# Kernel optimization log

Measured on AMD Instinct MI355X. Metric: run time of the kernel, lower is better.

Reference implementation:

```python
import jax, jax.numpy as jnp
import numpy as np

N_HEAD = 16
N_KV_HEAD = 4
HEAD_DIM = 64
VE_CH = 12  # min(12, n_embd)


def apply_rotary_emb(x, cos, sin):
    d = x.shape[3] // 2
    x1, x2 = x[..., :d], x[..., d:]
    return jnp.concatenate([x1 * cos + x2 * sin, x1 * -sin + x2 * cos], axis=3)


def rms_norm(x):
    return x * jax.lax.rsqrt(jnp.mean(jnp.square(x), axis=-1, keepdims=True) + 1e-6)


def setup_inputs() -> dict:
    key = jax.random.key(0)
    ks = jax.random.split(key, 9)
    B, T, C = 2, 2048, 1024
    s = 0.02
    return {
        "x": jax.random.normal(ks[0], (B, T, C), jnp.float32),
        "ve": jax.random.normal(ks[1], (B, T, N_KV_HEAD * HEAD_DIM), jnp.float32),
        "cos": jax.random.normal(ks[2], (1, T, 1, HEAD_DIM // 2), jnp.float32),
        "sin": jax.random.normal(ks[3], (1, T, 1, HEAD_DIM // 2), jnp.float32),
        "Wq": jax.random.normal(ks[4], (C, C), jnp.float32) * s,
        "Wk": jax.random.normal(ks[5], (N_KV_HEAD * HEAD_DIM, C), jnp.float32) * s,
        "Wv": jax.random.normal(ks[6], (N_KV_HEAD * HEAD_DIM, C), jnp.float32) * s,
        "Wo": jax.random.normal(ks[7], (C, C), jnp.float32) * s,
        "Wg": jax.random.normal(ks[8], (N_KV_HEAD, VE_CH), jnp.float32) * s,
    }


def reference(x, ve, cos, sin, Wq, Wk, Wv, Wo, Wg):
    B, T, C = x.shape
    q = (x @ Wq.T).reshape(B, T, N_HEAD, HEAD_DIM)
    k = (x @ Wk.T).reshape(B, T, N_KV_HEAD, HEAD_DIM)
    v = (x @ Wv.T).reshape(B, T, N_KV_HEAD, HEAD_DIM)

    # value-embedding gate
    ve_r = ve.reshape(B, T, N_KV_HEAD, HEAD_DIM)
    gate = 3.0 * jax.nn.sigmoid(x[..., :VE_CH] @ Wg.T)  # [B,T,n_kv_head]
    v = v + gate[..., None] * ve_r

    q = apply_rotary_emb(q, cos, sin)
    k = apply_rotary_emb(k, cos, sin)
    q = rms_norm(q) * 1.2
    k = rms_norm(k) * 1.2

    # GQA: expand kv heads
    r = N_HEAD // N_KV_HEAD
    k = jnp.repeat(k, r, axis=2)
    v = jnp.repeat(v, r, axis=2)

    # [B,H,T,D]
    q = q.transpose(0, 2, 1, 3)
    k = k.transpose(0, 2, 1, 3)
    v = v.transpose(0, 2, 1, 3)

    scale = 1.0 / np.sqrt(HEAD_DIM).astype(np.float32)
    scores = jnp.einsum("bhqd,bhkd->bhqk", q, k) * scale
    causal = jnp.tril(jnp.ones((T, T), dtype=bool))
    scores = jnp.where(causal, scores, jnp.float32(-jnp.inf))
    att = jax.nn.softmax(scores, axis=-1)
    y = jnp.einsum("bhqk,bhkd->bhqd", att, v)
    y = y.transpose(0, 2, 1, 3).reshape(B, T, C)
    return y @ Wo.T
```

## Files before the change

### kernel.cpp

```cpp
#include <hip/hip_runtime.h>
#include <stdint.h>

#define B_SZ 2
#define T_SZ 2048
#define C_SZ 1024
#define NH   16
#define NKV  4
#define HD   64
#define KVD  256
#define QKV_N 1536

typedef __attribute__((ext_vector_type(8))) short bf16x8;
typedef __attribute__((ext_vector_type(4))) float f32x4;

#define GL(p) ((const __attribute__((address_space(1))) void*)(p))
#define LD(p) ((__attribute__((address_space(3))) void*)(p))

__device__ inline unsigned short f2bf(float f) {
  union { float f; unsigned u; } v; v.f = f;
  unsigned u = v.u;
  unsigned r = (u + 0x7fffu + ((u >> 16) & 1u)) >> 16;
  return (unsigned short)r;
}
__device__ inline unsigned short bftrunc(float f) {
  union { float f; unsigned u; } v; v.f = f;
  return (unsigned short)(v.u >> 16);
}

struct Cvt5 {
  const float *s0, *s1, *s2, *s3, *s4;
  unsigned short *d0, *d1, *d2, *d3, *d4;
};
__global__ __launch_bounds__(256) void cvt_all(Cvt5 a) {
  int blk = blockIdx.x, tid = threadIdx.x;
  const float* s; unsigned short* d; int i;
  if      (blk < 4096) { s = a.s0; d = a.d0; i = blk * 256 + tid; }
  else if (blk < 5120) { s = a.s1; d = a.d1; i = (blk - 4096) * 256 + tid; }
  else if (blk < 5376) { s = a.s2; d = a.d2; i = (blk - 5120) * 256 + tid; }
  else if (blk < 5632) { s = a.s3; d = a.d3; i = (blk - 5376) * 256 + tid; }
  else                 { s = a.s4; d = a.d4; i = (blk - 5632) * 256 + tid; }
  float4 f = ((const float4*)s)[i];
  ushort4 o;
  o.x = f2bf(f.x); o.y = f2bf(f.y); o.z = f2bf(f.z); o.w = f2bf(f.w);
  ((ushort4*)d)[i] = o;
}

#define BM 64
#define BN 128
#define BK 32
__global__ __launch_bounds__(256) void gemm_bt(const unsigned short* __restrict__ A,
                                               const unsigned short* __restrict__ Bm,
                                               float* __restrict__ C,
                                               int M, int N, int K) {
  __shared__ unsigned short As[BM * BK];
  __shared__ unsigned short Bs[BN * BK];
  int tid  = threadIdx.x;
  int lane = tid & 63;
  int wave = tid >> 6;
  int quad = lane >> 4;
  int l16  = lane & 15;
  int m0 = blockIdx.y * BM;
  int n0 = blockIdx.x * BN;
  int wm = (wave & 1) * 32;
  int wn = (wave >> 1) * 64;

  f32x4 acc[2][4];
#pragma unroll
  for (int i = 0; i < 2; i++)
#pragma unroll
    for (int j = 0; j < 4; j++) acc[i][j] = (f32x4){0.f, 0.f, 0.f, 0.f};

  int srow = wave * 16;
  int lrow = lane >> 2;
  int lcol = (lane & 3) * 8;
  const unsigned short* aP  = &A[(size_t)(m0 + srow + lrow) * K + lcol];
  const unsigned short* b0P = &Bm[(size_t)(n0 + srow + lrow) * K + lcol];
  const unsigned short* b1P = b0P + 64 * (size_t)K;
  unsigned short* lA  = &As[srow * BK];
  unsigned short* lB0 = &Bs[srow * BK];
  unsigned short* lB1 = &Bs[(64 + srow) * BK];

  for (int k0 = 0; k0 < K; k0 += BK) {
    __syncthreads();
    __builtin_amdgcn_global_load_lds(GL(aP + k0),  LD(lA),  16, 0, 0);
    __builtin_amdgcn_global_load_lds(GL(b0P + k0), LD(lB0), 16, 0, 0);
    __builtin_amdgcn_global_load_lds(GL(b1P + k0), LD(lB1), 16, 0, 0);
    __syncthreads();

    bf16x8 af[2], bfr[4];
#pragma unroll
    for (int i = 0; i < 2; i++)
      af[i] = *(const bf16x8*)&As[(wm + i * 16 + l16) * BK + quad * 8];
#pragma unroll
    for (int j = 0; j < 4; j++)
      bfr[j] = *(const bf16x8*)&Bs[(wn + j * 16 + l16) * BK + quad * 8];
#pragma unroll
    for (int i = 0; i < 2; i++)
#pragma unroll
      for (int j = 0; j < 4; j++)
        acc[i][j] = __builtin_amdgcn_mfma_f32_16x16x32_bf16(af[i], bfr[j], acc[i][j], 0, 0, 0);
  }

#pragma unroll
  for (int i = 0; i < 2; i++) {
#pragma unroll
    for (int j = 0; j < 4; j++) {
      int col = n0 + wn + j * 16 + l16;
#pragma unroll
      for (int r = 0; r < 4; r++) {
        int row = m0 + wm + i * 16 + quad * 4 + r;
        C[(size_t)row * N + col] = acc[i][j][r];
      }
    }
  }
}

__global__ __launch_bounds__(256) void postproc(const float* __restrict__ qkv,
                                                const float* __restrict__ x,
                                                const float* __restrict__ ve,
                                                const float* __restrict__ cosb,
                                                const float* __restrict__ sinb,
                                                const float* __restrict__ Wg,
                                                unsigned short* __restrict__ qa,
                                                unsigned short* __restrict__ ka,
                                                unsigned short* __restrict__ vt) {
  int bt = blockIdx.x;
  int b = bt >> 11;
  int t = bt & 2047;
  int tid = threadIdx.x;
  __shared__ float row[QKV_N];
  __shared__ float gate[4];
  for (int i = tid; i < QKV_N; i += 256) row[i] = qkv[(size_t)bt * QKV_N + i];
  if (tid < 4) {
    float s = 0.f;
#pragma unroll
    for (int j = 0; j < 12; j++) s += x[(size_t)bt * C_SZ + j] * Wg[tid * 12 + j];
    gate[tid] = 3.f / (1.f + __expf(-s));
  }
  __syncthreads();

  int g = tid >> 3, sub = tid & 7;
  if (g < 20) {
    int off = (g < 16) ? g * 64 : 1024 + (g - 16) * 64;
    float o1[4], o2[4];
    float ssq = 0.f;
#pragma unroll
    for (int p = 0; p < 4; p++) {
      int j = sub * 4 + p;
      float cv = cosb[t * 32 + j];
      float sv = sinb[t * 32 + j];
      float a1 = row[off + j];
      float a2 = row[off + 32 + j];
      o1[p] = a1 * cv + a2 * sv;
      o2[p] = -a1 * sv + a2 * cv;
      ssq += o1[p] * o1[p] + o2[p] * o2[p];
    }
    ssq += __shfl_xor(ssq, 1);
    ssq += __shfl_xor(ssq, 2);
    ssq += __shfl_xor(ssq, 4);
    float rn = rsqrtf(ssq * (1.f / 64.f) + 1e-6f);
    rn *= (g < 16) ? (0.15f * 1.44269504088896f) : 1.2f;
    ushort4 w1, w2;
    w1.x = f2bf(o1[0] * rn); w1.y = f2bf(o1[1] * rn);
    w1.z = f2bf(o1[2] * rn); w1.w = f2bf(o1[3] * rn);
    w2.x = f2bf(o2[0] * rn); w2.y = f2bf(o2[1] * rn);
    w2.z = f2bf(o2[2] * rn); w2.w = f2bf(o2[3] * rn);
    if (g < 16) {
      size_t base = ((size_t)(b * NH + g) * T_SZ + t) * HD;
      *(ushort4*)&qa[base + sub * 4]      = w1;
      *(ushort4*)&qa[base + 32 + sub * 4] = w2;
    } else {
      size_t base = ((size_t)(b * NKV + (g - 16)) * T_SZ + t) * HD;
      *(ushort4*)&ka[base + sub * 4]      = w1;
      *(ushort4*)&ka[base + 32 + sub * 4] = w2;
    }
  }
  {
    int khh = tid >> 6, d = tid & 63;
    float val = row[1280 + tid] + gate[khh] * ve[(size_t)bt * KVD + tid];
    vt[((size_t)(b * NKV + khh) * HD + d) * T_SZ + t] = f2bf(val);
  }
}

#define KSTR 72
__global__ __launch_bounds__(256) void attn(const unsigned short* __restrict__ qa,
                                            const unsigned short* __restrict__ ka,
                                            const unsigned short* __restrict__ vt,
                                            unsigned short* __restrict__ y) {
  int bid = blockIdx.x;
  int half = bid >> 8, r = bid & 255;
  int qt = half ? (r & 15) : 15 - (r & 15);
  int bh = (half << 4) | (r >> 4);
  int b = bh >> 4, h = bh & 15;
  int kh = h >> 2;
  int tid = threadIdx.x;
  int wave = tid >> 6, lane = tid & 63;
  int quad = lane >> 4, l16 = lane & 15;

  __shared__ unsigned short Ks[64 * KSTR];
  __shared__ unsigned short Vs[64 * KSTR];
  __shared__ unsigned short Ps[128 * KSTR];
  unsigned short* Pw = &Ps[(wave * 32) * KSTR];

  bf16x8 aq[2][2];
#pragma unroll
  for (int mi = 0; mi < 2; mi++) {
    int tq = qt * 128 + wave * 32 + mi * 16 + l16;
    const unsigned short* qp = &qa[((size_t)(b * NH + h) * T_SZ + tq) * HD];
    aq[mi][0] = *(const bf16x8*)&qp[quad * 8];
    aq[mi][1] = *(const bf16x8*)&qp[32 + quad * 8];
  }

  const unsigned short one_bf = 0x3F80;
  bf16x8 vones = {(short)one_bf, (short)one_bf, (short)one_bf, (short)one_bf,
                  (short)one_bf, (short)one_bf, (short)one_bf, (short)one_bf};

  f32x4 oacc[2][4];
  f32x4 lacc[2];
#pragma unroll
  for (int mi = 0; mi < 2; mi++) {
    lacc[mi] = (f32x4){0.f, 0.f, 0.f, 0.f};
#pragma unroll
    for (int d = 0; d < 4; d++) oacc[mi][d] = (f32x4){0.f, 0.f, 0.f, 0.f};
  }

  int lr = tid >> 2;
  int lc = (tid & 3) * 16;

  const unsigned short* kbase = &ka[(size_t)(b * NKV + kh) * T_SZ * HD];
  const unsigned short* vbase = &vt[(size_t)(b * NKV + kh) * HD * T_SZ];

  int nj = 2 * qt + 2;

  uint4 k0, k1, v0, v1;
  {
    const unsigned short* kp = &kbase[(size_t)lr * HD + lc];
    const unsigned short* vp = &vbase[(size_t)lr * T_SZ + lc];
    k0 = *(const uint4*)(kp);
    k1 = *(const uint4*)(kp + 8);
    v0 = *(const uint4*)(vp);
    v1 = *(const uint4*)(vp + 8);
  }

  int qrow0 = qt * 128 + wave * 32;

  for (int j = 0; j < nj; j++) {
    __syncthreads();
    *(uint4*)&Ks[lr * KSTR + lc]     = k0;
    *(uint4*)&Ks[lr * KSTR + lc + 8] = k1;
    *(uint4*)&Vs[lr * KSTR + lc]     = v0;
    *(uint4*)&Vs[lr * KSTR + lc + 8] = v1;
    if (j + 1 < nj) {
      const unsigned short* kp = &kbase[(size_t)((j + 1) * 64 + lr) * HD + lc];
      const unsigned short* vp = &vbase[(size_t)lr * T_SZ + (j + 1) * 64 + lc];
      k0 = *(const uint4*)(kp);
      k1 = *(const uint4*)(kp + 8);
      v0 = *(const uint4*)(vp);
      v1 = *(const uint4*)(vp + 8);
    }
    __syncthreads();

    f32x4 sa[2][4];
#pragma unroll
    for (int nb = 0; nb < 4; nb++) {
      bf16x8 bk0 = *(const bf16x8*)&Ks[(nb * 16 + l16) * KSTR + quad * 8];
      bf16x8 bk1 = *(const bf16x8*)&Ks[(nb * 16 + l16) * KSTR + 32 + quad * 8];
#pragma unroll
      for (int mi = 0; mi < 2; mi++) {
        f32x4 s = (f32x4){0.f, 0.f, 0.f, 0.f};
        s = __builtin_amdgcn_mfma_f32_16x16x32_bf16(aq[mi][0], bk0, s, 0, 0, 0);
        s = __builtin_amdgcn_mfma_f32_16x16x32_bf16(aq[mi][1], bk1, s, 0, 0, 0);
        sa[mi][nb] = s;
      }
    }

#pragma unroll
    for (int mi = 0; mi < 2; mi++) {
      int rowLow = qrow0 + mi * 16;
      if (j * 64 + 63 > rowLow) {
#pragma unroll
        for (int nb = 0; nb < 4; nb++) {
          int col = j * 64 + nb * 16 + l16;
#pragma unroll
          for (int i = 0; i < 4; i++) {
            if (col > rowLow + quad * 4 + i) sa[mi][nb][i] = -__builtin_inff();
          }
        }
      }
    }

#pragma unroll
    for (int mi = 0; mi < 2; mi++)
#pragma unroll
      for (int nb = 0; nb < 4; nb++)
#pragma unroll
        for (int i = 0; i < 4; i++)
          Pw[(mi * 16 + quad * 4 + i) * KSTR + nb * 16 + l16] =
              bftrunc(__builtin_amdgcn_exp2f(sa[mi][nb][i]));

    bf16x8 ap[2][2];
#pragma unroll
    for (int mi = 0; mi < 2; mi++) {
      ap[mi][0] = *(const bf16x8*)&Pw[(mi * 16 + l16) * KSTR + quad * 8];
      ap[mi][1] = *(const bf16x8*)&Pw[(mi * 16 + l16) * KSTR + 32 + quad * 8];
      lacc[mi] = __builtin_amdgcn_mfma_f32_16x16x32_bf16(ap[mi][0], vones, lacc[mi], 0, 0, 0);
      lacc[mi] = __builtin_amdgcn_mfma_f32_16x16x32_bf16(ap[mi][1], vones, lacc[mi], 0, 0, 0);
    }
#pragma unroll
    for (int d = 0; d < 4; d++) {
      bf16x8 bv0 = *(const bf16x8*)&Vs[(d * 16 + l16) * KSTR + quad * 8];
      bf16x8 bv1 = *(const bf16x8*)&Vs[(d * 16 + l16) * KSTR + 32 + quad * 8];
#pragma unroll
      for (int mi = 0; mi < 2; mi++) {
        oacc[mi][d] = __builtin_amdgcn_mfma_f32_16x16x32_bf16(ap[mi][0], bv0, oacc[mi][d], 0, 0, 0);
        oacc[mi][d] = __builtin_amdgcn_mfma_f32_16x16x32_bf16(ap[mi][1], bv1, oacc[mi][d], 0, 0, 0);
      }
    }
  }

#pragma unroll
  for (int mi = 0; mi < 2; mi++) {
#pragma unroll
    for (int i = 0; i < 4; i++) {
      int tq = qrow0 + mi * 16 + quad * 4 + i;
      float inv = 1.f / lacc[mi][i];
#pragma unroll
      for (int d = 0; d < 4; d++) {
        y[((size_t)(b * T_SZ) + tq) * C_SZ + h * HD + d * 16 + l16] = f2bf(oacc[mi][d][i] * inv);
      }
    }
  }
}

extern "C" void kernel_launch(void* const* d_in, const int* in_sizes, int n_in,
                              void* d_out, int out_size, void* d_ws, size_t ws_size,
                              hipStream_t stream) {
  const float* x    = (const float*)d_in[0];
  const float* ve   = (const float*)d_in[1];
  const float* cosb = (const float*)d_in[2];
  const float* sinb = (const float*)d_in[3];
  const float* Wq   = (const float*)d_in[4];
  const float* Wk   = (const float*)d_in[5];
  const float* Wv   = (const float*)d_in[6];
  const float* Wo   = (const float*)d_in[7];
  const float* Wg   = (const float*)d_in[8];
  float* out = (float*)d_out;

  const size_t MB = 1024 * 1024;
  char* ws = (char*)d_ws;
  unsigned short* xb    = (unsigned short*)(ws);
  unsigned short* wqkvb = (unsigned short*)(ws + 8 * MB);
  unsigned short* wob   = (unsigned short*)(ws + 11 * MB);
  float*          qkvf  = (float*)(ws + 13 * MB);
  unsigned short* qab   = (unsigned short*)(ws + 37 * MB);
  unsigned short* kab   = (unsigned short*)(ws + 45 * MB);
  unsigned short* vtb   = (unsigned short*)(ws + 47 * MB);
  unsigned short* yb    = xb;

  Cvt5 ca;
  ca.s0 = x;  ca.d0 = xb;
  ca.s1 = Wq; ca.d1 = wqkvb;
  ca.s2 = Wk; ca.d2 = wqkvb + 1024 * 1024;
  ca.s3 = Wv; ca.d3 = wqkvb + 1280 * 1024;
  ca.s4 = Wo; ca.d4 = wob;
  cvt_all<<<6656, 256, 0, stream>>>(ca);

  gemm_bt<<<dim3(QKV_N / BN, (B_SZ * T_SZ) / BM), 256, 0, stream>>>(
      xb, wqkvb, qkvf, B_SZ * T_SZ, QKV_N, C_SZ);

  postproc<<<B_SZ * T_SZ, 256, 0, stream>>>(qkvf, x, ve, cosb, sinb, Wg, qab, kab, vtb);

  attn<<<512, 256, 0, stream>>>(qab, kab, vtb, yb);

  gemm_bt<<<dim3(C_SZ / BN, (B_SZ * T_SZ) / BM), 256, 0, stream>>>(
      yb, wob, out, B_SZ * T_SZ, C_SZ, C_SZ);
}
```

Baseline: 199.2 us.

## Fuse rotary, RMS norm and value gating into QKV GEMM epilogue

Removes the separate postproc kernel and the fp32 QKV intermediate buffer. The QKV GEMM epilogue now applies rotary embedding, RMS norm and scaling per head, and adds the gated value embedding before writing bf16 Q, K and transposed V directly. The gate sigmoid is computed by extra blocks in the conversion kernel. The GEMM main loop now loads a 64-wide K slice per barrier pair, as two 32-wide buffers, to halve synchronisation. In exchange the epilogue uses scattered 2-byte stores and the transposed V writes are strided.

```diff
diff --git a/kernel.cpp b/kernel.cpp
--- a/kernel.cpp
+++ b/kernel.cpp
@@ -27,12 +27,23 @@
   return (unsigned short)(v.u >> 16);
 }
 
-struct Cvt5 {
+struct CvtArgs {
   const float *s0, *s1, *s2, *s3, *s4;
   unsigned short *d0, *d1, *d2, *d3, *d4;
+  const float *x, *Wg;
+  float *gate;
 };
-__global__ __launch_bounds__(256) void cvt_all(Cvt5 a) {
+__global__ __launch_bounds__(256) void cvt_all(CvtArgs a) {
   int blk = blockIdx.x, tid = threadIdx.x;
+  if (blk >= 6656) {
+    int idx = (blk - 6656) * 256 + tid;
+    int bt = idx >> 2, kh = idx & 3;
+    float s = 0.f;
+#pragma unroll
+    for (int j = 0; j < 12; j++) s += a.x[(size_t)bt * C_SZ + j] * a.Wg[kh * 12 + j];
+    a.gate[idx] = 3.f / (1.f + __expf(-s));
+    return;
+  }
   const float* s; unsigned short* d; int i;
   if      (blk < 4096) { s = a.s0; d = a.d0; i = blk * 256 + tid; }
   else if (blk < 5120) { s = a.s1; d = a.d1; i = (blk - 4096) * 256 + tid; }
@@ -47,60 +58,54 @@
 
 #define BM 64
 #define BN 128
-#define BK 32
+#define GEMM_PROLOG(A, Bm, K)                                                        \
+  __shared__ unsigned short As[2][BM * 32];                                          \
+  __shared__ unsigned short Bs[2][BN * 32];                                          \
+  int tid  = threadIdx.x;                                                            \
+  int lane = tid & 63;                                                               \
+  int wave = tid >> 6;                                                               \
+  int quad = lane >> 4;                                                              \
+  int l16  = lane & 15;                                                              \
+  int m0 = blockIdx.y * BM;                                                          \
+  int n0 = blockIdx.x * BN;                                                          \
+  int wm = (wave & 1) * 32;                                                          \
+  int wn = (wave >> 1) * 64;                                                         \
+  f32x4 acc[2][4];                                                                   \
+  _Pragma("unroll") for (int i = 0; i < 2; i++)                                      \
+    _Pragma("unroll") for (int j = 0; j < 4; j++)                                    \
+      acc[i][j] = (f32x4){0.f, 0.f, 0.f, 0.f};                                       \
+  int lrow = lane >> 2;                                                              \
+  int lcol = (lane & 3) * 8;                                                         \
+  int srowA = wave * 16;                                                             \
+  int srowB = wave * 32;                                                             \
+  const unsigned short* aP  = &A[(size_t)(m0 + srowA + lrow) * K + lcol];            \
+  const unsigned short* b0P = &Bm[(size_t)(n0 + srowB + lrow) * K + lcol];           \
+  const unsigned short* b1P = b0P + 16 * (size_t)K;                                  \
+  for (int k0 = 0; k0 < K; k0 += 64) {                                               \
+    __syncthreads();                                                                 \
+    _Pragma("unroll") for (int p = 0; p < 2; p++) {                                  \
+      __builtin_amdgcn_global_load_lds(GL(aP  + k0 + p * 32), LD(&As[p][srowA * 32]), 16, 0, 0); \
+      __builtin_amdgcn_global_load_lds(GL(b0P + k0 + p * 32), LD(&Bs[p][srowB * 32]), 16, 0, 0); \
+      __builtin_amdgcn_global_load_lds(GL(b1P + k0 + p * 32), LD(&Bs[p][(srowB + 16) * 32]), 16, 0, 0); \
+    }                                                                                \
+    __syncthreads();                                                                 \
+    _Pragma("unroll") for (int p = 0; p < 2; p++) {                                  \
+      bf16x8 af[2], bfr[4];                                                          \
+      _Pragma("unroll") for (int i = 0; i < 2; i++)                                  \
+        af[i] = *(const bf16x8*)&As[p][(wm + i * 16 + l16) * 32 + quad * 8];         \
+      _Pragma("unroll") for (int j = 0; j < 4; j++)                                  \
+        bfr[j] = *(const bf16x8*)&Bs[p][(wn + j * 16 + l16) * 32 + quad * 8];        \
+      _Pragma("unroll") for (int i = 0; i < 2; i++)                                  \
+        _Pragma("unroll") for (int j = 0; j < 4; j++)                                \
+          acc[i][j] = __builtin_amdgcn_mfma_f32_16x16x32_bf16(af[i], bfr[j], acc[i][j], 0, 0, 0); \
+    }                                                                                \
+  }
+
 __global__ __launch_bounds__(256) void gemm_bt(const unsigned short* __restrict__ A,
                                                const unsigned short* __restrict__ Bm,
                                                float* __restrict__ C,
-                                               int M, int N, int K) {
-  __shared__ unsigned short As[BM * BK];
-  __shared__ unsigned short Bs[BN * BK];
-  int tid  = threadIdx.x;
-  int lane = tid & 63;
-  int wave = tid >> 6;
-  int quad = lane >> 4;
-  int l16  = lane & 15;
-  int m0 = blockIdx.y * BM;
-  int n0 = blockIdx.x * BN;
-  int wm = (wave & 1) * 32;
-  int wn = (wave >> 1) * 64;
-
-  f32x4 acc[2][4];
-#pragma unroll
-  for (int i = 0; i < 2; i++)
-#pragma unroll
-    for (int j = 0; j < 4; j++) acc[i][j] = (f32x4){0.f, 0.f, 0.f, 0.f};
-
-  int srow = wave * 16;
-  int lrow = lane >> 2;
-  int lcol = (lane & 3) * 8;
-  const unsigned short* aP  = &A[(size_t)(m0 + srow + lrow) * K + lcol];
-  const unsigned short* b0P = &Bm[(size_t)(n0 + srow + lrow) * K + lcol];
-  const unsigned short* b1P = b0P + 64 * (size_t)K;
-  unsigned short* lA  = &As[srow * BK];
-  unsigned short* lB0 = &Bs[srow * BK];
-  unsigned short* lB1 = &Bs[(64 + srow) * BK];
-
-  for (int k0 = 0; k0 < K; k0 += BK) {
-    __syncthreads();
-    __builtin_amdgcn_global_load_lds(GL(aP + k0),  LD(lA),  16, 0, 0);
-    __builtin_amdgcn_global_load_lds(GL(b0P + k0), LD(lB0), 16, 0, 0);
-    __builtin_amdgcn_global_load_lds(GL(b1P + k0), LD(lB1), 16, 0, 0);
-    __syncthreads();
-
-    bf16x8 af[2], bfr[4];
-#pragma unroll
-    for (int i = 0; i < 2; i++)
-      af[i] = *(const bf16x8*)&As[(wm + i * 16 + l16) * BK + quad * 8];
-#pragma unroll
-    for (int j = 0; j < 4; j++)
-      bfr[j] = *(const bf16x8*)&Bs[(wn + j * 16 + l16) * BK + quad * 8];
-#pragma unroll
-    for (int i = 0; i < 2; i++)
-#pragma unroll
-      for (int j = 0; j < 4; j++)
-        acc[i][j] = __builtin_amdgcn_mfma_f32_16x16x32_bf16(af[i], bfr[j], acc[i][j], 0, 0, 0);
-  }
-
+                                               int N, int K) {
+  GEMM_PROLOG(A, Bm, K)
 #pragma unroll
   for (int i = 0; i < 2; i++) {
 #pragma unroll
@@ -115,70 +120,70 @@
   }
 }
 
-__global__ __launch_bounds__(256) void postproc(const float* __restrict__ qkv,
-                                                const float* __restrict__ x,
+__global__ __launch_bounds__(256) void gemm_qkv(const unsigned short* __restrict__ A,
+                                                const unsigned short* __restrict__ Bm,
                                                 const float* __restrict__ ve,
                                                 const float* __restrict__ cosb,
                                                 const float* __restrict__ sinb,
-                                                const float* __restrict__ Wg,
+                                                const float* __restrict__ gateArr,
                                                 unsigned short* __restrict__ qa,
                                                 unsigned short* __restrict__ ka,
                                                 unsigned short* __restrict__ vt) {
-  int bt = blockIdx.x;
-  int b = bt >> 11;
-  int t = bt & 2047;
-  int tid = threadIdx.x;
-  __shared__ float row[QKV_N];
-  __shared__ float gate[4];
-  for (int i = tid; i < QKV_N; i += 256) row[i] = qkv[(size_t)bt * QKV_N + i];
-  if (tid < 4) {
-    float s = 0.f;
-#pragma unroll
-    for (int j = 0; j < 12; j++) s += x[(size_t)bt * C_SZ + j] * Wg[tid * 12 + j];
-    gate[tid] = 3.f / (1.f + __expf(-s));
-  }
-  __syncthreads();
-
-  int g = tid >> 3, sub = tid & 7;
-  if (g < 20) {
-    int off = (g < 16) ? g * 64 : 1024 + (g - 16) * 64;
-    float o1[4], o2[4];
-    float ssq = 0.f;
-#pragma unroll
-    for (int p = 0; p < 4; p++) {
-      int j = sub * 4 + p;
-      float cv = cosb[t * 32 + j];
-      float sv = sinb[t * 32 + j];
-      float a1 = row[off + j];
-      float a2 = row[off + 32 + j];
-      o1[p] = a1 * cv + a2 * sv;
-      o2[p] = -a1 * sv + a2 * cv;
-      ssq += o1[p] * o1[p] + o2[p] * o2[p];
-    }
-    ssq += __shfl_xor(ssq, 1);
-    ssq += __shfl_xor(ssq, 2);
-    ssq += __shfl_xor(ssq, 4);
-    float rn = rsqrtf(ssq * (1.f / 64.f) + 1e-6f);
-    rn *= (g < 16) ? (0.15f * 1.44269504088896f) : 1.2f;
-    ushort4 w1, w2;
-    w1.x = f2bf(o1[0] * rn); w1.y = f2bf(o1[1] * rn);
-    w1.z = f2bf(o1[2] * rn); w1.w = f2bf(o1[3] * rn);
-    w2.x = f2bf(o2[0] * rn); w2.y = f2bf(o2[1] * rn);
-    w2.z = f2bf(o2[2] * rn); w2.w = f2bf(o2[3] * rn);
-    if (g < 16) {
-      size_t base = ((size_t)(b * NH + g) * T_SZ + t) * HD;
-      *(ushort4*)&qa[base + sub * 4]      = w1;
-      *(ushort4*)&qa[base + 32 + sub * 4] = w2;
-    } else {
-      size_t base = ((size_t)(b * NKV + (g - 16)) * T_SZ + t) * HD;
-      *(ushort4*)&ka[base + sub * 4]      = w1;
-      *(ushort4*)&ka[base + 32 + sub * 4] = w2;
-    }
-  }
-  {
-    int khh = tid >> 6, d = tid & 63;
-    float val = row[1280 + tid] + gate[khh] * ve[(size_t)bt * KVD + tid];
-    vt[((size_t)(b * NKV + khh) * HD + d) * T_SZ + t] = f2bf(val);
+  const int K = C_SZ;
+  GEMM_PROLOG(A, Bm, K)
+
+  int colbase = n0 + wn;
+  if (colbase < 1280) {
+    int isQ = colbase < 1024;
+    int h   = isQ ? (colbase >> 6) : ((colbase - 1024) >> 6);
+    float scale = isQ ? (0.15f * 1.44269504088896f) : 1.2f;
+    unsigned short* dst = isQ ? qa : ka;
+    int nheads = isQ ? NH : NKV;
+#pragma unroll
+    for (int i = 0; i < 2; i++) {
+#pragma unroll
+      for (int r = 0; r < 4; r++) {
+        int row = m0 + wm + i * 16 + quad * 4 + r;
+        int t = row & (T_SZ - 1), b = row >> 11;
+        float a10 = acc[i][0][r], a11 = acc[i][1][r];
+        float a20 = acc[i][2][r], a21 = acc[i][3][r];
+        float cv0 = cosb[t * 32 + l16],      sv0 = sinb[t * 32 + l16];
+        float cv1 = cosb[t * 32 + 16 + l16], sv1 = sinb[t * 32 + 16 + l16];
+        float o10 =  a10 * cv0 + a20 * sv0;
+        float o11 =  a11 * cv1 + a21 * sv1;
+        float o20 = -a10 * sv0 + a20 * cv0;
+        float o21 = -a11 * sv1 + a21 * cv1;
+        float ssq = o10 * o10 + o11 * o11 + o20 * o20 + o21 * o21;
+        ssq += __shfl_xor(ssq, 1);
+        ssq += __shfl_xor(ssq, 2);
+        ssq += __shfl_xor(ssq, 4);
+        ssq += __shfl_xor(ssq, 8);
+        float rn = rsqrtf(ssq * (1.f / 64.f) + 1e-6f) * scale;
+        size_t base = ((size_t)(b * nheads + h) * T_SZ + t) * HD;
+        dst[base + l16]      = f2bf(o10 * rn);
+        dst[base + 16 + l16] = f2bf(o11 * rn);
+        dst[base + 32 + l16] = f2bf(o20 * rn);
+        dst[base + 48 + l16] = f2bf(o21 * rn);
+      }
+    }
+  } else {
+    int kh = (colbase - 1280) >> 6;
+#pragma unroll
+    for (int i = 0; i < 2; i++) {
+#pragma unroll
+      for (int r = 0; r < 4; r++) {
+        int row = m0 + wm + i * 16 + quad * 4 + r;
+        int t = row & (T_SZ - 1), b = row >> 11;
+        float g = gateArr[row * 4 + kh];
+        size_t vbase = ((size_t)(b * NKV + kh) * HD) * T_SZ;
+#pragma unroll
+        for (int j = 0; j < 4; j++) {
+          int d = j * 16 + l16;
+          float val = acc[i][j][r] + g * ve[(size_t)row * KVD + kh * HD + d];
+          vt[vbase + (size_t)d * T_SZ + t] = f2bf(val);
+        }
+      }
+    }
   }
 }
 
@@ -351,27 +356,26 @@
   unsigned short* xb    = (unsigned short*)(ws);
   unsigned short* wqkvb = (unsigned short*)(ws + 8 * MB);
   unsigned short* wob   = (unsigned short*)(ws + 11 * MB);
-  float*          qkvf  = (float*)(ws + 13 * MB);
-  unsigned short* qab   = (unsigned short*)(ws + 37 * MB);
-  unsigned short* kab   = (unsigned short*)(ws + 45 * MB);
-  unsigned short* vtb   = (unsigned short*)(ws + 47 * MB);
+  unsigned short* qab   = (unsigned short*)(ws + 13 * MB);
+  unsigned short* kab   = (unsigned short*)(ws + 21 * MB);
+  unsigned short* vtb   = (unsigned short*)(ws + 23 * MB);
+  float*          gateA = (float*)(ws + 25 * MB);
   unsigned short* yb    = xb;
 
-  Cvt5 ca;
+  CvtArgs ca;
   ca.s0 = x;  ca.d0 = xb;
   ca.s1 = Wq; ca.d1 = wqkvb;
   ca.s2 = Wk; ca.d2 = wqkvb + 1024 * 1024;
   ca.s3 = Wv; ca.d3 = wqkvb + 1280 * 1024;
   ca.s4 = Wo; ca.d4 = wob;
-  cvt_all<<<6656, 256, 0, stream>>>(ca);
-
-  gemm_bt<<<dim3(QKV_N / BN, (B_SZ * T_SZ) / BM), 256, 0, stream>>>(
-      xb, wqkvb, qkvf, B_SZ * T_SZ, QKV_N, C_SZ);
-
-  postproc<<<B_SZ * T_SZ, 256, 0, stream>>>(qkvf, x, ve, cosb, sinb, Wg, qab, kab, vtb);
+  ca.x = x; ca.Wg = Wg; ca.gate = gateA;
+  cvt_all<<<6720, 256, 0, stream>>>(ca);
+
+  gemm_qkv<<<dim3(QKV_N / BN, (B_SZ * T_SZ) / BM), 256, 0, stream>>>(
+      xb, wqkvb, ve, cosb, sinb, gateA, qab, kab, vtb);
 
   attn<<<512, 256, 0, stream>>>(qab, kab, vtb, yb);
 
   gemm_bt<<<dim3(C_SZ / BN, (B_SZ * T_SZ) / BM), 256, 0, stream>>>(
-      yb, wob, out, B_SZ * T_SZ, C_SZ, C_SZ);
-}
+      yb, wob, out, C_SZ, C_SZ);
+}
```

Measured after the change: 179.8 us. 9.7% less time.
